# Performance work log

Hardware: AMD Instinct MI355X
Metric: run time of the kernel (lower is better)

## Reference

```python
import jax, jax.numpy as jnp
import numpy as np

N_TOKENS = 16384
HIDDEN = 4096
N_EXPERTS = 64
TOP_K = 8


def setup_inputs() -> dict:
    key = jax.random.key(0)
    kx, kw, kb = jax.random.split(key, 3)
    x = jax.random.normal(kx, (N_TOKENS, HIDDEN), dtype=jnp.float32)
    # nn.Linear(hidden_dim, expert_num): weight [E, H], bias [E]
    W = jax.random.normal(kw, (N_EXPERTS, HIDDEN), dtype=jnp.float32) * (1.0 / np.sqrt(HIDDEN))
    b = jax.random.normal(kb, (N_EXPERTS,), dtype=jnp.float32) * 0.01
    return {"x": x, "W": W, "b": b}


def reference(x, W, b):
    # gate linear: [N, H] @ [H, E] + [E] -> [N, E]
    router = jnp.einsum("nh,eh->ne", x, W) + b
    # softmax over experts
    router_logits = jax.nn.softmax(router, axis=-1)
    # top-k over experts: values/indices [N, K]
    top_k_logits, top_k_indices = jax.lax.top_k(router_logits, TOP_K)
    # renormalize the selected probs
    router_weight = top_k_logits / jnp.sum(top_k_logits, axis=-1, keepdims=True)
    router_weight = router_weight.astype(x.dtype)
    # one-hot mask [N, K, E] -> permute(2,1,0) -> [E, K, N]
    expert_mask = jax.nn.one_hot(top_k_indices, N_EXPERTS, dtype=jnp.int32)
    expert_mask = jnp.transpose(expert_mask, (2, 1, 0))
    return (router, router_weight, top_k_indices, expert_mask)
```

## Files before the change

### kernel.cpp

```cpp
#include <hip/hip_runtime.h>

#define N_TOK 16384
#define HID   4096
#define N_EXP 64
#define TOPK  8

#define OFF_WT   (N_TOK * N_EXP)
#define OFF_IDX  (OFF_WT + N_TOK * TOPK)
#define OFF_MASK (OFF_IDX + N_TOK * TOPK)

typedef __attribute__((ext_vector_type(8))) _Float16 f16x8;
typedef __attribute__((ext_vector_type(4))) float f32x4;

static __device__ __forceinline__ void hsplit(float f, unsigned short &h, unsigned short &l)
{
    _Float16 hh = (_Float16)f;
    float r = f - (float)hh;
    _Float16 hl = (_Float16)r;
    h = __builtin_bit_cast(unsigned short, hh);
    l = __builtin_bit_cast(unsigned short, hl);
}

__global__ __launch_bounds__(256)
void prep_w(const float* __restrict__ W,
            unsigned short* __restrict__ wh, unsigned short* __restrict__ wl)
{
    const int i = blockIdx.x * 256 + threadIdx.x;
    float4 f = ((const float4*)W)[i];
    unsigned short h0,l0,h1,l1,h2,l2,h3,l3;
    hsplit(f.x,h0,l0); hsplit(f.y,h1,l1); hsplit(f.z,h2,l2); hsplit(f.w,h3,l3);
    *(uint2*)&wh[4*i] = make_uint2((unsigned)h0 | ((unsigned)h1<<16), (unsigned)h2 | ((unsigned)h3<<16));
    *(uint2*)&wl[4*i] = make_uint2((unsigned)l0 | ((unsigned)l1<<16), (unsigned)l2 | ((unsigned)l3<<16));
}

__global__ __launch_bounds__(256, 4)
void router_gemm(const float* __restrict__ x,
                 const unsigned short* __restrict__ wh,
                 const unsigned short* __restrict__ wl,
                 const float* __restrict__ b,
                 float* __restrict__ router)
{
    const int tid  = threadIdx.x;
    const int lane = tid & 63, wv = tid >> 6;
    const long t0  = (long)blockIdx.x * 16;
    const int  e0  = wv * 16;
    const int  lrow = lane & 15, lg = lane >> 4;

    const float*          xp  = x  + (t0 + lrow) * (long)HID + lg * 8;
    const unsigned short* whp = wh + (long)(e0 + lrow) * HID + lg * 8;
    const unsigned short* wlp = wl + (long)(e0 + lrow) * HID + lg * 8;

    f32x4 acc = {};

    auto LOAD = [&](int st, float4 (&xv)[4], uint4 (&hv)[2], uint4 (&lv)[2]) {
        const long o = (long)st * 64;
        xv[0] = *(const float4*)(xp + o);
        xv[1] = *(const float4*)(xp + o + 4);
        xv[2] = *(const float4*)(xp + o + 32);
        xv[3] = *(const float4*)(xp + o + 36);
        hv[0] = *(const uint4*)(whp + o);
        hv[1] = *(const uint4*)(whp + o + 32);
        lv[0] = *(const uint4*)(wlp + o);
        lv[1] = *(const uint4*)(wlp + o + 32);
    };

    auto COMP = [&](const float4 (&xv)[4], const uint4 (&hv)[2], const uint4 (&lv)[2]) {
#pragma unroll
        for (int ks = 0; ks < 2; ++ks) {
            float xf[8];
            *(float4*)&xf[0] = xv[2 * ks];
            *(float4*)&xf[4] = xv[2 * ks + 1];
            f16x8 ah, al;
#pragma unroll
            for (int j = 0; j < 8; ++j) {
                _Float16 h = (_Float16)xf[j];
                ah[j] = h;
                al[j] = (_Float16)(xf[j] - (float)h);
            }
            const f16x8 bh = __builtin_bit_cast(f16x8, hv[ks]);
            const f16x8 bl = __builtin_bit_cast(f16x8, lv[ks]);
            acc = __builtin_amdgcn_mfma_f32_16x16x32_f16(ah, bh, acc, 0, 0, 0);
            acc = __builtin_amdgcn_mfma_f32_16x16x32_f16(ah, bl, acc, 0, 0, 0);
            acc = __builtin_amdgcn_mfma_f32_16x16x32_f16(al, bh, acc, 0, 0, 0);
        }
    };

    float4 xA[4], xB[4];
    uint4  hA[2], hB[2], lA[2], lB[2];

    LOAD(0, xA, hA, lA);
    LOAD(1, xB, hB, lB);

#pragma unroll 1
    for (int st = 0; st < HID / 64; st += 2) {
        COMP(xA, hA, lA);
        if (st + 2 < HID / 64) LOAD(st + 2, xA, hA, lA);
        COMP(xB, hB, lB);
        if (st + 3 < HID / 64) LOAD(st + 3, xB, hB, lB);
    }

    const int e = e0 + lrow;
    const float bias = b[e];
#pragma unroll
    for (int r = 0; r < 4; ++r) {
        const long tok = t0 + lg * 4 + r;
        router[tok * N_EXP + e] = acc[r] + bias;
    }
}

__global__ __launch_bounds__(256)
void router_topk(const float* __restrict__ router, float* __restrict__ out)
{
    const int tid  = threadIdx.x;
    const int lane = tid & 63;
    const int wv   = tid >> 6;
    const int n    = blockIdx.x * 4 + wv;

    float l = router[(long)n * N_EXP + lane];

    float m = l;
#pragma unroll
    for (int o = 32; o > 0; o >>= 1) m = fmaxf(m, __shfl_xor(m, o));
    float p = expf(l - m);
    float Z = p;
#pragma unroll
    for (int o = 32; o > 0; o >>= 1) Z += __shfl_xor(Z, o);
    float prob = p / Z;

    float cur = prob;
    float myv = 0.f;
    int   myi = 0;
    float ssum = 0.f;
#pragma unroll
    for (int k = 0; k < TOPK; ++k) {
        float v = cur;
        int   id = lane;
#pragma unroll
        for (int o = 32; o > 0; o >>= 1) {
            float ov = __shfl_xor(v, o);
            int   oi = __shfl_xor(id, o);
            if (ov > v || (ov == v && oi < id)) { v = ov; id = oi; }
        }
        if (lane == k)  { myv = v; myi = id; }
        if (lane == id) cur = -1.f;
        ssum += v;
    }

    if (lane < TOPK) {
        out[OFF_WT  + (long)n * TOPK + lane] = myv / ssum;
        out[OFF_IDX + (long)n * TOPK + lane] = (float)myi;
    }
}

__global__ __launch_bounds__(256)
void mask_fill(const float* __restrict__ idxf, float* __restrict__ mask)
{
    const int bid = blockIdx.x;
    const int ek  = bid >> 2, qtr = bid & 3;
    const int k   = ek & 7;
    const float fe = (float)(ek >> 3);
    float* mbase = mask + (long)ek * N_TOK;
#pragma unroll
    for (int j = 0; j < 4; ++j) {
        const int n = qtr * 4096 + j * 1024 + threadIdx.x * 4;
        float4 v;
        v.x = (idxf[(long)(n + 0) * TOPK + k] == fe) ? 1.f : 0.f;
        v.y = (idxf[(long)(n + 1) * TOPK + k] == fe) ? 1.f : 0.f;
        v.z = (idxf[(long)(n + 2) * TOPK + k] == fe) ? 1.f : 0.f;
        v.w = (idxf[(long)(n + 3) * TOPK + k] == fe) ? 1.f : 0.f;
        *(float4*)&mbase[n] = v;
    }
}

extern "C" void kernel_launch(void* const* d_in, const int* in_sizes, int n_in,
                              void* d_out, int out_size, void* d_ws, size_t ws_size,
                              hipStream_t stream)
{
    const float* x = (const float*)d_in[0];
    const float* W = (const float*)d_in[1];
    const float* b = (const float*)d_in[2];
    float* out = (float*)d_out;

    unsigned short* wsh = (unsigned short*)d_ws;
    unsigned short* wsl = wsh + (size_t)N_EXP * HID;

    hipLaunchKernelGGL(prep_w,      dim3(N_EXP * HID / 1024), dim3(256), 0, stream, W, wsh, wsl);
    hipLaunchKernelGGL(router_gemm, dim3(N_TOK / 16),         dim3(256), 0, stream, x, wsh, wsl, b, out);
    hipLaunchKernelGGL(router_topk, dim3(N_TOK / 4),          dim3(256), 0, stream, out, out);
    hipLaunchKernelGGL(mask_fill,   dim3(N_EXP * TOPK * 4),   dim3(256), 0, stream,
                       out + OFF_IDX, out + OFF_MASK);
}
```

Baseline: 541.7 us.

## Stage x and W tiles through swizzled LDS with double buffering in router GEMM

The router GEMM now loads each 16-token x tile and the 64-expert W chunk cooperatively into double-buffered shared memory. The x fp16 hi/lo split is done once per element at store time instead of being repeated by each of the 4 waves, and an XOR swizzle is applied to avoid LDS bank conflicts. Before, every wave re-read the same x rows from global memory and re-split them. The cost is a __syncthreads per 64-wide K step, more LDS traffic, and a lower occupancy hint (2 blocks per CU instead of 4).

```diff
diff --git a/kernel.cpp b/kernel.cpp
--- a/kernel.cpp
+++ b/kernel.cpp
@@ -4,6 +4,10 @@
 #define HID   4096
 #define N_EXP 64
 #define TOPK  8
+
+#define CH    64
+#define NST   (HID / CH)
+#define TT    16
 
 #define OFF_WT   (N_TOK * N_EXP)
 #define OFF_IDX  (OFF_WT + N_TOK * TOPK)
@@ -33,70 +37,89 @@
     *(uint2*)&wl[4*i] = make_uint2((unsigned)l0 | ((unsigned)l1<<16), (unsigned)l2 | ((unsigned)l3<<16));
 }
 
-__global__ __launch_bounds__(256, 4)
+__global__ __launch_bounds__(256, 2)
 void router_gemm(const float* __restrict__ x,
                  const unsigned short* __restrict__ wh,
                  const unsigned short* __restrict__ wl,
                  const float* __restrict__ b,
                  float* __restrict__ router)
 {
-    const int tid  = threadIdx.x;
+    __shared__ unsigned short sXh[2][TT * CH];
+    __shared__ unsigned short sXl[2][TT * CH];
+    __shared__ unsigned short sWh[2][N_EXP * CH];
+    __shared__ unsigned short sWl[2][N_EXP * CH];
+
+    const int tid = threadIdx.x;
+    const long t0 = (long)blockIdx.x * TT;
+
+    const int xr = tid >> 4, xc = tid & 15;
+    const int wr = tid >> 2, wc = tid & 3;
+
+    const float*          xb  = x  + (t0 + xr) * (long)HID + xc * 4;
+    const unsigned short* whb = wh + (long)wr * HID + wc * 16;
+    const unsigned short* wlb = wl + (long)wr * HID + wc * 16;
+
     const int lane = tid & 63, wv = tid >> 6;
-    const long t0  = (long)blockIdx.x * 16;
-    const int  e0  = wv * 16;
-    const int  lrow = lane & 15, lg = lane >> 4;
-
-    const float*          xp  = x  + (t0 + lrow) * (long)HID + lg * 8;
-    const unsigned short* whp = wh + (long)(e0 + lrow) * HID + lg * 8;
-    const unsigned short* wlp = wl + (long)(e0 + lrow) * HID + lg * 8;
-
+    const int e0 = wv * 16;
+    const int lrow = lane & 15, lg = lane >> 4, sw = lane & 7;
+
+    float4 gx; uint4 gwh[2], gwl[2];
     f32x4 acc = {};
 
-    auto LOAD = [&](int st, float4 (&xv)[4], uint4 (&hv)[2], uint4 (&lv)[2]) {
-        const long o = (long)st * 64;
-        xv[0] = *(const float4*)(xp + o);
-        xv[1] = *(const float4*)(xp + o + 4);
-        xv[2] = *(const float4*)(xp + o + 32);
-        xv[3] = *(const float4*)(xp + o + 36);
-        hv[0] = *(const uint4*)(whp + o);
-        hv[1] = *(const uint4*)(whp + o + 32);
-        lv[0] = *(const uint4*)(wlp + o);
-        lv[1] = *(const uint4*)(wlp + o + 32);
+    auto LOAD = [&](int st) {
+        const long o = (long)st * CH;
+        gx = *(const float4*)(xb + o);
+#pragma unroll
+        for (int j = 0; j < 2; ++j) {
+            gwh[j] = *(const uint4*)(whb + o + j * 8);
+            gwl[j] = *(const uint4*)(wlb + o + j * 8);
+        }
     };
 
-    auto COMP = [&](const float4 (&xv)[4], const uint4 (&hv)[2], const uint4 (&lv)[2]) {
+    auto STORE = [&](int buf) {
+        {
+            const int q = xc >> 1;
+            const int a = xr * CH + (((q ^ (xr & 7)) << 3) | ((xc & 1) << 2));
+            unsigned short h0,l0,h1,l1,h2,l2,h3,l3;
+            hsplit(gx.x,h0,l0); hsplit(gx.y,h1,l1);
+            hsplit(gx.z,h2,l2); hsplit(gx.w,h3,l3);
+            *(uint2*)&sXh[buf][a] = make_uint2((unsigned)h0 | ((unsigned)h1<<16), (unsigned)h2 | ((unsigned)h3<<16));
+            *(uint2*)&sXl[buf][a] = make_uint2((unsigned)l0 | ((unsigned)l1<<16), (unsigned)l2 | ((unsigned)l3<<16));
+        }
+#pragma unroll
+        for (int j = 0; j < 2; ++j) {
+            const int q = wc * 2 + j;
+            const int a = wr * CH + ((q ^ (wr & 7)) << 3);
+            *(uint4*)&sWh[buf][a] = gwh[j];
+            *(uint4*)&sWl[buf][a] = gwl[j];
+        }
+    };
+
+    auto COMPUTE = [&](int buf) {
 #pragma unroll
         for (int ks = 0; ks < 2; ++ks) {
-            float xf[8];
-            *(float4*)&xf[0] = xv[2 * ks];
-            *(float4*)&xf[4] = xv[2 * ks + 1];
-            f16x8 ah, al;
-#pragma unroll
-            for (int j = 0; j < 8; ++j) {
-                _Float16 h = (_Float16)xf[j];
-                ah[j] = h;
-                al[j] = (_Float16)(xf[j] - (float)h);
-            }
-            const f16x8 bh = __builtin_bit_cast(f16x8, hv[ks]);
-            const f16x8 bl = __builtin_bit_cast(f16x8, lv[ks]);
+            const int qs = ((ks * 4 + lg) ^ sw) << 3;
+            const int aA = lrow * CH + qs;
+            const int aB = (e0 + lrow) * CH + qs;
+            f16x8 ah = *(const f16x8*)&sXh[buf][aA];
+            f16x8 al = *(const f16x8*)&sXl[buf][aA];
+            f16x8 bh = *(const f16x8*)&sWh[buf][aB];
+            f16x8 bl = *(const f16x8*)&sWl[buf][aB];
             acc = __builtin_amdgcn_mfma_f32_16x16x32_f16(ah, bh, acc, 0, 0, 0);
             acc = __builtin_amdgcn_mfma_f32_16x16x32_f16(ah, bl, acc, 0, 0, 0);
             acc = __builtin_amdgcn_mfma_f32_16x16x32_f16(al, bh, acc, 0, 0, 0);
         }
     };
 
-    float4 xA[4], xB[4];
-    uint4  hA[2], hB[2], lA[2], lB[2];
-
-    LOAD(0, xA, hA, lA);
-    LOAD(1, xB, hB, lB);
-
+    LOAD(0);
+    STORE(0);
+    __syncthreads();
 #pragma unroll 1
-    for (int st = 0; st < HID / 64; st += 2) {
-        COMP(xA, hA, lA);
-        if (st + 2 < HID / 64) LOAD(st + 2, xA, hA, lA);
-        COMP(xB, hB, lB);
-        if (st + 3 < HID / 64) LOAD(st + 3, xB, hB, lB);
+    for (int st = 0; st < NST; ++st) {
+        if (st + 1 < NST) LOAD(st + 1);
+        COMPUTE(st & 1);
+        if (st + 1 < NST) STORE((st + 1) & 1);
+        __syncthreads();
     }
 
     const int e = e0 + lrow;
@@ -185,7 +208,7 @@
     unsigned short* wsl = wsh + (size_t)N_EXP * HID;
 
     hipLaunchKernelGGL(prep_w,      dim3(N_EXP * HID / 1024), dim3(256), 0, stream, W, wsh, wsl);
-    hipLaunchKernelGGL(router_gemm, dim3(N_TOK / 16),         dim3(256), 0, stream, x, wsh, wsl, b, out);
+    hipLaunchKernelGGL(router_gemm, dim3(N_TOK / TT),         dim3(256), 0, stream, x, wsh, wsl, b, out);
     hipLaunchKernelGGL(router_topk, dim3(N_TOK / 4),          dim3(256), 0, stream, out, out);
     hipLaunchKernelGGL(mask_fill,   dim3(N_EXP * TOPK * 4),   dim3(256), 0, stream,
                        out + OFF_IDX, out + OFF_MASK);
```

Result: slower. 683.0 us (+26.1%).
